# Kernel optimization log

Hardware: AMD Instinct MI355X
Metric: run time of the kernel (lower is better)

## Reference

```python
import jax, jax.numpy as jnp
import numpy as np

D_MODEL = 1024
D_STATE = 8          # max(8, 16 // 2)
D_CONV = 4
D_INNER = int(1.5 * D_MODEL)   # expand = max(1.5, 2*0.75)
DT_RANK = (D_MODEL + 15) // 16 # 64
D_FF = 2 * D_MODEL
B, L = 2, 2048


def layer_norm(x, g, b, eps=1e-5):
    mu = jnp.mean(x, -1, keepdims=True)
    var = jnp.var(x, -1, keepdims=True)
    return (x - mu) * jax.lax.rsqrt(var + eps) * g + b


def setup_inputs() -> dict:
    key = jax.random.key(0)
    ks = jax.random.split(key, 12)
    def n(k, shape, scale=0.02):
        return jax.random.normal(k, shape, dtype=jnp.float32) * scale
    return {
        'x': jax.random.normal(ks[0], (B, L, D_MODEL), dtype=jnp.float32),
        'ln1_g': jnp.ones((D_MODEL,), jnp.float32),
        'ln1_b': jnp.zeros((D_MODEL,), jnp.float32),
        'ln2_g': jnp.ones((D_MODEL,), jnp.float32),
        'ln2_b': jnp.zeros((D_MODEL,), jnp.float32),
        'in_proj_w': n(ks[1], (2 * D_INNER, D_MODEL)),
        'conv_w': n(ks[2], (D_INNER, 1, D_CONV), 0.1),
        'conv_b': jnp.zeros((D_INNER,), jnp.float32),
        'x_proj_w': n(ks[3], (DT_RANK + 2 * D_STATE, D_INNER)),
        'dt_proj_w': n(ks[4], (D_INNER, DT_RANK), 0.1),
        'dt_proj_b': n(ks[5], (D_INNER,), 0.1),
        'A_log': jnp.log(jnp.broadcast_to(jnp.arange(1, D_STATE + 1, dtype=jnp.float32), (D_INNER, D_STATE))),
        'D': jnp.ones((D_INNER,), jnp.float32),
        'out_proj_w': n(ks[6], (D_MODEL, D_INNER)),
        'ffn_w1': n(ks[7], (D_FF, D_MODEL)),
        'ffn_b1': jnp.zeros((D_FF,), jnp.float32),
        'ffn_w2': n(ks[8], (D_MODEL, D_FF)),
        'ffn_b2': jnp.zeros((D_MODEL,), jnp.float32),
    }


def mamba(x, in_proj_w, conv_w, conv_b, x_proj_w, dt_proj_w, dt_proj_b, A_log, Dp, out_proj_w):
    # in_proj -> (x, z)
    xz = x @ in_proj_w.T                       # (B, L, 2*d_inner)
    xi, z = jnp.split(xz, 2, axis=-1)
    # depthwise causal conv over seq, kernel 4
    xc = jnp.transpose(xi, (0, 2, 1))          # (B, d_inner, L)
    xc = jax.lax.conv_general_dilated(
        xc, conv_w, window_strides=(1,), padding=[(D_CONV - 1, 0)],
        dimension_numbers=('NCH', 'OIH', 'NCH'), feature_group_count=D_INNER)
    xc = xc + conv_b[None, :, None]
    u = jax.nn.silu(jnp.transpose(xc, (0, 2, 1)))  # (B, L, d_inner)
    # x_proj -> dt, B, C
    x_dbl = u @ x_proj_w.T
    dt = x_dbl[..., :DT_RANK]
    Bm = x_dbl[..., DT_RANK:DT_RANK + D_STATE]
    Cm = x_dbl[..., DT_RANK + D_STATE:]
    delta = jax.nn.softplus(dt @ dt_proj_w.T + dt_proj_b)  # (B, L, d_inner)
    A = -jnp.exp(A_log)                                    # (d_inner, d_state)
    dA = jnp.exp(jnp.einsum('bld,dn->bldn', delta, A))     # (B, L, d_inner, d_state)
    dBu = jnp.einsum('bld,bln,bld->bldn', delta, Bm, u)
    # selective scan over time
    def step(h, inputs):
        dA_t, dBu_t, C_t = inputs
        h = dA_t * h + dBu_t                   # (B, d_inner, d_state)
        y = jnp.einsum('bdn,bn->bd', h, C_t)
        return h, y
    h0 = jnp.zeros((x.shape[0], D_INNER, D_STATE), x.dtype)
    _, ys = jax.lax.scan(step, h0, (jnp.moveaxis(dA, 1, 0), jnp.moveaxis(dBu, 1, 0), jnp.moveaxis(Cm, 1, 0)))
    y = jnp.moveaxis(ys, 0, 1) + u * Dp        # skip connection D*u
    y = y * jax.nn.silu(z)                     # gate
    return y @ out_proj_w.T


def reference(x, ln1_g, ln1_b, ln2_g, ln2_b, in_proj_w, conv_w, conv_b, x_proj_w,
              dt_proj_w, dt_proj_b, A_log, D, out_proj_w, ffn_w1, ffn_b1, ffn_w2, ffn_b2):
    residual = x
    xp = layer_norm(x, ln1_g, ln1_b)
    x = mamba(xp, in_proj_w, conv_w, conv_b, x_proj_w, dt_proj_w, dt_proj_b, A_log, D, out_proj_w) + residual
    xn = layer_norm(x, ln2_g, ln2_b)
    h = jax.nn.gelu(xn @ ffn_w1.T + ffn_b1, approximate=False)  # dropout is identity in eval
    return x + (h @ ffn_w2.T + ffn_b2)
```

## Files before the change

### kernel.cpp

```cpp
#include <hip/hip_runtime.h>
#include <math.h>

#define D_MODEL 1024
#define D_STATE 8
#define D_CONV  4
#define D_INNER 1536
#define DT_RANK 64
#define D_FF    2048
#define BATCH   2
#define SEQ     2048
#define NROWS   (BATCH*SEQ)
#define NC      32
#define LC      (SEQ/NC)
#define XPAD    128

typedef short bf16x8 __attribute__((ext_vector_type(8)));
typedef unsigned short u16x8 __attribute__((ext_vector_type(8)));
typedef float f32x4  __attribute__((ext_vector_type(4)));

__device__ inline unsigned short f2bf(float x) {
    union { float f; unsigned u; } v; v.f = x;
    unsigned r = v.u + 0x7fffu + ((v.u >> 16) & 1u);
    return (unsigned short)(r >> 16);
}
__device__ inline float bf2f(unsigned short h) {
    union { unsigned u; float f; } v; v.u = ((unsigned)h) << 16;
    return v.f;
}
__device__ inline float softplus_f(float x) {
    return (x > 20.0f) ? x : log1pf(__expf(x));
}
__device__ inline float gelu_f(float x) {
    return 0.5f * x * (1.0f + erff(x * 0.70710678118654752f));
}
__device__ inline float silu_f(float x) {
    return x / (1.0f + __expf(-x));
}
__device__ inline void gload16(const unsigned short* g, unsigned short* l) {
    typedef unsigned int u32;
    __builtin_amdgcn_global_load_lds(
        (const __attribute__((address_space(1))) u32*)g,
        (__attribute__((address_space(3))) u32*)l, 16, 0, 0);
}

#define PHASE_SYNC_PRE()  do { __builtin_amdgcn_s_barrier(); \
                               asm volatile("s_waitcnt lgkmcnt(0)" ::: "memory"); } while (0)
#define PHASE_SYNC_POST() do { __builtin_amdgcn_s_barrier(); } while (0)

__global__ __launch_bounds__(256) void prep_kernel(
    const float* __restrict__ s0, unsigned short* __restrict__ d0,
    const float* __restrict__ s1, unsigned short* __restrict__ d1,
    const float* __restrict__ s2, unsigned short* __restrict__ d2,
    const float* __restrict__ s3, unsigned short* __restrict__ d3,
    const float* __restrict__ s4, unsigned short* __restrict__ d4,
    const float* __restrict__ xpw, unsigned short* __restrict__ xpd,
    const float* __restrict__ x, const float* __restrict__ g1,
    const float* __restrict__ b1, unsigned short* __restrict__ xout) {
    int b = blockIdx.x;
    if (b < 4400) {
        const float* s; unsigned short* d; int base;
        if      (b < 1536) { s = s0; d = d0; base = b * 2048; }
        else if (b < 1584) { s = s1; d = d1; base = (b - 1536) * 2048; }
        else if (b < 2352) { s = s2; d = d2; base = (b - 1584) * 2048; }
        else if (b < 3376) { s = s3; d = d3; base = (b - 2352) * 2048; }
        else               { s = s4; d = d4; base = (b - 3376) * 2048; }
        int i = base + threadIdx.x * 8;
        float4 v0 = *(const float4*)(s + i);
        float4 v1 = *(const float4*)(s + i + 4);
        ushort4 a, c;
        a.x = f2bf(v0.x); a.y = f2bf(v0.y); a.z = f2bf(v0.z); a.w = f2bf(v0.w);
        c.x = f2bf(v1.x); c.y = f2bf(v1.y); c.z = f2bf(v1.z); c.w = f2bf(v1.w);
        *(ushort4*)(d + i)     = a;
        *(ushort4*)(d + i + 4) = c;
    } else if (b < 4528) {
        int row = b - 4400;
        for (int c = threadIdx.x; c < D_INNER; c += 256)
            xpd[row * D_INNER + c] = (row < 80) ? f2bf(xpw[row * D_INNER + c]) : (unsigned short)0;
    } else {
        __shared__ float sbuf[4];
        int row = b - 4528;
        int t = threadIdx.x;
        float4 v = ((const float4*)(x + (size_t)row * D_MODEL))[t];
        float s = v.x + v.y + v.z + v.w;
        for (int o = 32; o; o >>= 1) s += __shfl_down(s, o, 64);
        if ((t & 63) == 0) sbuf[t >> 6] = s;
        __syncthreads();
        float mu = (sbuf[0] + sbuf[1] + sbuf[2] + sbuf[3]) * (1.0f / D_MODEL);
        __syncthreads();
        float e0 = v.x - mu, e1 = v.y - mu, e2 = v.z - mu, e3 = v.w - mu;
        float q = e0*e0 + e1*e1 + e2*e2 + e3*e3;
        for (int o = 32; o; o >>= 1) q += __shfl_down(q, o, 64);
        if ((t & 63) == 0) sbuf[t >> 6] = q;
        __syncthreads();
        float var = (sbuf[0] + sbuf[1] + sbuf[2] + sbuf[3]) * (1.0f / D_MODEL);
        float rs = rsqrtf(var + 1e-5f);
        float4 gv = ((const float4*)g1)[t];
        float4 bv = ((const float4*)b1)[t];
        ushort4 st;
        st.x = f2bf(e0 * rs * gv.x + bv.x);
        st.y = f2bf(e1 * rs * gv.y + bv.y);
        st.z = f2bf(e2 * rs * gv.z + bv.z);
        st.w = f2bf(e3 * rs * gv.w + bv.w);
        ((ushort4*)(xout + (size_t)row * D_MODEL))[t] = st;
    }
}

__global__ __launch_bounds__(256) void ln_kernel(const float* __restrict__ x,
                                                 const float* __restrict__ g,
                                                 const float* __restrict__ b,
                                                 unsigned short* __restrict__ out) {
    __shared__ float sbuf[4];
    int row = blockIdx.x;
    int t = threadIdx.x;
    float4 v = ((const float4*)(x + (size_t)row * D_MODEL))[t];
    float s = v.x + v.y + v.z + v.w;
    for (int o = 32; o; o >>= 1) s += __shfl_down(s, o, 64);
    if ((t & 63) == 0) sbuf[t >> 6] = s;
    __syncthreads();
    float mu = (sbuf[0] + sbuf[1] + sbuf[2] + sbuf[3]) * (1.0f / D_MODEL);
    __syncthreads();
    float d0 = v.x - mu, d1 = v.y - mu, d2 = v.z - mu, d3 = v.w - mu;
    float q = d0*d0 + d1*d1 + d2*d2 + d3*d3;
    for (int o = 32; o; o >>= 1) q += __shfl_down(q, o, 64);
    if ((t & 63) == 0) sbuf[t >> 6] = q;
    __syncthreads();
    float var = (sbuf[0] + sbuf[1] + sbuf[2] + sbuf[3]) * (1.0f / D_MODEL);
    float rs = rsqrtf(var + 1e-5f);
    float4 gv = ((const float4*)g)[t];
    float4 bv = ((const float4*)b)[t];
    ushort4 st;
    st.x = f2bf(d0 * rs * gv.x + bv.x);
    st.y = f2bf(d1 * rs * gv.y + bv.y);
    st.z = f2bf(d2 * rs * gv.z + bv.z);
    st.w = f2bf(d3 * rs * gv.w + bv.w);
    ((ushort4*)(out + (size_t)row * D_MODEL))[t] = st;
}

#define EPI_F32        0
#define EPI_F32_BF16   1
#define EPI_SOFTPLUS   2
#define EPI_RESID      3
#define EPI_GELU_BF16  4
#define EPI_BIAS_RESID 5
#define EPI_BF16       6
#define EPI_SOFTPLUS_BF16 7

template<int WN, int EPI, int SPLITK>
__global__ __launch_bounds__(512, 2) void gemm8p(
    const unsigned short* __restrict__ A, int lda,
    const unsigned short* __restrict__ Bm, int ldb, int K,
    float* __restrict__ Cf, unsigned short* __restrict__ Cb, int ldc,
    const float* __restrict__ bias,
    const float* __restrict__ resid, int ldr) {
    constexpr int WM = 8 / WN;
    constexpr int BN = WN * 64;
    constexpr int RW = 256 / WM;
    constexpr int CW = 64;
    constexpr int MI = RW / 16;
    constexpr int NI = CW / 16;
    constexpr int MIH = MI / 2, NIH = NI / 2;
    constexpr int ABYTES = 256 * 128;
    constexpr int BBYTES = BN * 128;
    constexpr int BOFF = 2 * ABYTES;
    __shared__ unsigned short lds[(2 * ABYTES + 2 * BBYTES) / 2];

    const int t = threadIdx.x, l = t & 63, w = t >> 6;
    const int wr = w / WN, wc = w % WN;

    const int nx = gridDim.x;
    const int nwg = nx * gridDim.y;
    int bid = blockIdx.y * nx + blockIdx.x;
    int q = nwg >> 3;
    int swz = (bid & 7) * q + (bid >> 3);
    const int m0 = (swz / nx) * 256, n0 = (swz % nx) * BN;
    const int kbase = (SPLITK > 1) ? blockIdx.z * K : 0;

    const int sr = l >> 3;
    const int sj = ((l & 7) * 16) ^ ((l >> 3) << 4);
    const int row_l = w * 8;
    const int row_c = (w >> 2) * 64 + (w & 3) * 8;

    auto STG = [&](int bufbyte, int rowbase, const unsigned short* G, int ldg, int gbase, int kt) {
        unsigned short* dst = (unsigned short*)((char*)lds + bufbyte + rowbase * 128);
        const unsigned short* src = G + (size_t)(gbase + rowbase + sr) * ldg + kbase + kt * 64 + (sj >> 1);
        gload16(src, dst);
    };
    auto S_Ah0 = [&](int b, int kt) {
        if (WN == 4) { STG(b * ABYTES, row_l, A, lda, m0, kt);       STG(b * ABYTES, 128 + row_l, A, lda, m0, kt); }
        else         { STG(b * ABYTES, row_c, A, lda, m0, kt);       STG(b * ABYTES, 128 + row_c, A, lda, m0, kt); }
    };
    auto S_Ah1 = [&](int b, int kt) {
        if (WN == 4) { STG(b * ABYTES, 64 + row_l, A, lda, m0, kt);  STG(b * ABYTES, 192 + row_l, A, lda, m0, kt); }
        else         { STG(b * ABYTES, 32 + row_c, A, lda, m0, kt);  STG(b * ABYTES, 160 + row_c, A, lda, m0, kt); }
    };
    auto S_Bc0 = [&](int b, int kt) {
        if (WN == 4) { STG(BOFF + b * BBYTES, row_c, Bm, ldb, n0, kt); STG(BOFF + b * BBYTES, 128 + row_c, Bm, ldb, n0, kt); }
        else         { STG(BOFF + b * BBYTES, row_c, Bm, ldb, n0, kt); }
    };
    auto S_Bc1 = [&](int b, int kt) {
        if (WN == 4) { STG(BOFF + b * BBYTES, 32 + row_c, Bm, ldb, n0, kt); STG(BOFF + b * BBYTES, 160 + row_c, Bm, ldb, n0, kt); }
        else         { STG(BOFF + b * BBYTES, 32 + row_c, Bm, ldb, n0, kt); }
    };

    auto LD = [&](int bytebase, int row, int kb) -> bf16x8 {
        int o = bytebase + row * 128 + (kb ^ ((row & 7) << 4));
        return *(const bf16x8*)((const char*)lds + o);
    };

    f32x4 acc[MI][NI] = {};
    bf16x8 af[MIH][2], b0v[NIH][2], b1v[NIH][2];

    auto LDA_set = [&](int buf, int qr, auto& dst) {
        #pragma unroll
        for (int mi = 0; mi < MIH; mi++)
            #pragma unroll
            for (int ks = 0; ks < 2; ks++)
                dst[mi][ks] = LD(buf * ABYTES, wr * RW + qr * (RW / 2) + mi * 16 + (l & 15),
                                 ks * 64 + (l >> 4) * 16);
    };
    auto LDB_set = [&](int buf, int qc, auto& dst) {
        #pragma unroll
        for (int ni2 = 0; ni2 < NIH; ni2++)
            #pragma unroll
            for (int ks = 0; ks < 2; ks++)
                dst[ni2][ks] = LD(BOFF + buf * BBYTES, wc * CW + qc * 32 + ni2 * 16 + (l & 15),
                                  ks * 64 + (l >> 4) * 16);
    };
    auto MFMA_Q = [&](int qr, int qc, auto& a_, auto& b_) {
        __builtin_amdgcn_s_setprio(1);
        #pragma unroll
        for (int mi = 0; mi < MIH; mi++)
            #pragma unroll
            for (int ni2 = 0; ni2 < NIH; ni2++)
                #pragma unroll
                for (int ks = 0; ks < 2; ks++)
                    acc[qr * MIH + mi][qc * NIH + ni2] =
                        __builtin_amdgcn_mfma_f32_16x16x32_bf16(a_[mi][ks], b_[ni2][ks],
                                                                acc[qr * MIH + mi][qc * NIH + ni2], 0, 0, 0);
        __builtin_amdgcn_s_setprio(0);
    };
    auto VMW = [&](bool last) {
        if (last)            asm volatile("s_waitcnt vmcnt(0)" ::: "memory");
        else if (WN == 4)    asm volatile("s_waitcnt vmcnt(6)" ::: "memory");
        else                 asm volatile("s_waitcnt vmcnt(5)" ::: "memory");
    };

    const int ni_ = K >> 7;

    S_Ah0(0, 0); S_Ah1(0, 0); S_Bc0(0, 0); S_Bc1(0, 0);
    S_Ah0(1, 1); S_Ah1(1, 1); S_Bc0(1, 1); S_Bc1(1, 1);
    if (WN == 4) asm volatile("s_waitcnt vmcnt(8)" ::: "memory");
    else         asm volatile("s_waitcnt vmcnt(6)" ::: "memory");
    __builtin_amdgcn_s_barrier();

    for (int i = 0; i < ni_; i++) {
        const bool last = (i == ni_ - 1);
        const int t2 = 2 * i + 2, t3 = 2 * i + 3;
        LDA_set(0, 0, af); LDB_set(0, 0, b0v);
        if (i) S_Bc0(1, 2 * i + 1);
        PHASE_SYNC_PRE(); MFMA_Q(0, 0, af, b0v); PHASE_SYNC_POST();
        LDB_set(0, 1, b1v);
        if (!last) S_Ah0(0, t2);
        PHASE_SYNC_PRE(); MFMA_Q(0, 1, af, b1v); PHASE_SYNC_POST();
        LDA_set(0, 1, af);
        PHASE_SYNC_PRE(); MFMA_Q(1, 1, af, b1v); PHASE_SYNC_POST();
        LDB_set(0, 0, b0v);
        if (!last) { S_Ah1(0, t2); S_Bc1(0, t2); }
        VMW(last);
        PHASE_SYNC_PRE(); MFMA_Q(1, 0, af, b0v); PHASE_SYNC_POST();
        LDA_set(1, 0, af); LDB_set(1, 0, b0v);
        if (!last) S_Bc0(0, t2);
        PHASE_SYNC_PRE(); MFMA_Q(0, 0, af, b0v); PHASE_SYNC_POST();
        LDB_set(1, 1, b1v);
        if (!last) S_Ah0(1, t3);
        PHASE_SYNC_PRE(); MFMA_Q(0, 1, af, b1v); PHASE_SYNC_POST();
        LDA_set(1, 1, af);
        PHASE_SYNC_PRE(); MFMA_Q(1, 1, af, b1v); PHASE_SYNC_POST();
        LDB_set(1, 0, b0v);
        if (!last) { S_Ah1(1, t3); S_Bc1(1, t3); }
        VMW(last);
        PHASE_SYNC_PRE(); MFMA_Q(1, 0, af, b0v); PHASE_SYNC_POST();
    }

    float* Cfp = Cf;
    if (SPLITK > 1) Cfp += (size_t)blockIdx.z * NROWS * ldc;
    #pragma unroll
    for (int ni2 = 0; ni2 < NI; ni2++) {
        int col = n0 + wc * CW + ni2 * 16 + (l & 15);
        float bv = 0.0f;
        if (EPI == EPI_SOFTPLUS || EPI == EPI_GELU_BF16 || EPI == EPI_BIAS_RESID) bv = bias[col];
        #pragma unroll
        for (int mi = 0; mi < MI; mi++) {
            #pragma unroll
            for (int j = 0; j < 4; j++) {
                int row = m0 + wr * RW + mi * 16 + (l >> 4) * 4 + j;
                float v = acc[mi][ni2][j];
                if (EPI == EPI_SOFTPLUS)        v = softplus_f(v + bv);
                else if (EPI == EPI_GELU_BF16)  v = gelu_f(v + bv);
                else if (EPI == EPI_RESID)      v = v + resid[(size_t)row * ldr + col];
                else if (EPI == EPI_BIAS_RESID) v = v + bv + resid[(size_t)row * ldr + col];
                if (EPI == EPI_GELU_BF16 || EPI == EPI_BF16) {
                    Cb[(size_t)row * ldc + col] = f2bf(v);
                } else {
                    Cfp[(size_t)row * ldc + col] = v;
                    if (EPI == EPI_F32_BF16) Cb[(size_t)row * ldc + col] = f2bf(v);
                }
            }
        }
    }
}

__global__ __launch_bounds__(256) void sk2_ln(const float* __restrict__ p,
                                              const float* __restrict__ resid,
                                              const float* __restrict__ g,
                                              const float* __restrict__ b,
                                              float* __restrict__ x2,
                                              unsigned short* __restrict__ xn) {
    __shared__ float sbuf[4];
    int row = blockIdx.x;
    int t = threadIdx.x;
    const size_t seg = (size_t)NROWS * D_MODEL;
    size_t base = (size_t)row * D_MODEL + t * 4;
    float4 a = *(const float4*)(p + base);
    float4 bb = *(const float4*)(p + base + seg);
    float4 r = *(const float4*)(resid + base);
    float4 v;
    v.x = a.x + bb.x + r.x;
    v.y = a.y + bb.y + r.y;
    v.z = a.z + bb.z + r.z;
    v.w = a.w + bb.w + r.w;
    *(float4*)(x2 + base) = v;
    float s = v.x + v.y + v.z + v.w;
    for (int o = 32; o; o >>= 1) s += __shfl_down(s, o, 64);
    if ((t & 63) == 0) sbuf[t >> 6] = s;
    __syncthreads();
    float mu = (sbuf[0] + sbuf[1] + sbuf[2] + sbuf[3]) * (1.0f / D_MODEL);
    __syncthreads();
    float d0 = v.x - mu, d1 = v.y - mu, d2 = v.z - mu, d3 = v.w - mu;
    float qq = d0*d0 + d1*d1 + d2*d2 + d3*d3;
    for (int o = 32; o; o >>= 1) qq += __shfl_down(qq, o, 64);
    if ((t & 63) == 0) sbuf[t >> 6] = qq;
    __syncthreads();
    float var = (sbuf[0] + sbuf[1] + sbuf[2] + sbuf[3]) * (1.0f / D_MODEL);
    float rs = rsqrtf(var + 1e-5f);
    float4 gv = ((const float4*)g)[t];
    float4 bv = ((const float4*)b)[t];
    ushort4 st;
    st.x = f2bf(d0 * rs * gv.x + bv.x);
    st.y = f2bf(d1 * rs * gv.y + bv.y);
    st.z = f2bf(d2 * rs * gv.z + bv.z);
    st.w = f2bf(d3 * rs * gv.w + bv.w);
    ((ushort4*)(xn + (size_t)row * D_MODEL))[t] = st;
}

__global__ __launch_bounds__(256) void sk2_reduce(const float* __restrict__ p,
                                                  const float* __restrict__ bias,
                                                  const float* __restrict__ resid,
                                                  float* __restrict__ o) {
    int i = (blockIdx.x * 256 + threadIdx.x) * 4;
    const size_t seg = (size_t)NROWS * D_MODEL;
    float4 a = *(const float4*)(p + i);
    float4 b = *(const float4*)(p + i + seg);
    float4 r = *(const float4*)(resid + i);
    float4 bb = *(const float4*)(bias + (i & (D_MODEL - 1)));
    float4 o4;
    o4.x = a.x + b.x + r.x + bb.x;
    o4.y = a.y + b.y + r.y + bb.y;
    o4.z = a.z + b.z + r.z + bb.z;
    o4.w = a.w + b.w + r.w + bb.w;
    *(float4*)(o + i) = o4;
}

template<int EPI, int SPLITK>
__global__ __launch_bounds__(256) void gemm_mfma(
    const unsigned short* __restrict__ A, int lda,
    const unsigned short* __restrict__ B, int ldb, int K,
    float* __restrict__ Cf, unsigned short* __restrict__ Cb, int ldc,
    const float* __restrict__ bias,
    const float* __restrict__ resid, int ldr) {
    __shared__ unsigned short As[3][128 * 32];
    __shared__ unsigned short Bs[3][128 * 32];
    int t = threadIdx.x, l = t & 63, w = t >> 6;
    int nx = gridDim.x;
    int nwg = nx * gridDim.y;
    int bid = blockIdx.y * nx + blockIdx.x;
    int q = nwg >> 3;
    int swz = (bid & 7) * q + (bid >> 3);
    int m0 = (swz / nx) * 128, n0 = (swz % nx) * 128;
    int kbase = (SPLITK > 1) ? blockIdx.z * K : 0;
    int c0 = 2 * w, c1 = 2 * w + 1;
    int srow = l >> 2, scol = (l & 3) * 8;
    const unsigned short* Ag0 = A + (size_t)(m0 + 16 * c0 + srow) * lda + kbase + scol;
    const unsigned short* Ag1 = A + (size_t)(m0 + 16 * c1 + srow) * lda + kbase + scol;
    const unsigned short* Bg0 = B + (size_t)(n0 + 16 * c0 + srow) * ldb + kbase + scol;
    const unsigned short* Bg1 = B + (size_t)(n0 + 16 * c1 + srow) * ldb + kbase + scol;
    int wr = w >> 1, wc = w & 1;
    int aoff = (wr * 64 + (l & 15)) * 32 + (l >> 4) * 8;
    int boff = (wc * 64 + (l & 15)) * 32 + (l >> 4) * 8;

    f32x4 acc[4][4] = {};
    int nt = K >> 5;

    gload16(Ag0, &As[0][c0 * 512]);
    gload16(Ag1, &As[0][c1 * 512]);
    gload16(Bg0, &Bs[0][c0 * 512]);
    gload16(Bg1, &Bs[0][c1 * 512]);
    if (nt > 1) {
        gload16(Ag0 + 32, &As[1][c0 * 512]);
        gload16(Ag1 + 32, &As[1][c1 * 512]);
        gload16(Bg0 + 32, &Bs[1][c0 * 512]);
        gload16(Bg1 + 32, &Bs[1][c1 * 512]);
    }

    int cur = 0;
    for (int ti = 0; ti < nt; ti++) {
        int pf = ti + 2;
        if (pf < nt) {
            int nb = cur - 1; if (nb < 0) nb += 3;
            int k0 = pf << 5;
            gload16(Ag0 + k0, &As[nb][c0 * 512]);
            gload16(Ag1 + k0, &As[nb][c1 * 512]);
            gload16(Bg0 + k0, &Bs[nb][c0 * 512]);
            gload16(Bg1 + k0, &Bs[nb][c1 * 512]);
        }
        int rem = nt - 1 - ti;
        if (rem >= 2)      asm volatile("s_waitcnt vmcnt(8)" ::: "memory");
        else if (rem == 1) asm volatile("s_waitcnt vmcnt(4)" ::: "memory");
        else               asm volatile("s_waitcnt vmcnt(0)" ::: "memory");
        __builtin_amdgcn_s_barrier();

        const unsigned short* Ab = &As[cur][0];
        const unsigned short* Bb = &Bs[cur][0];
        bf16x8 af[4], bfv[4];
        #pragma unroll
        for (int i = 0; i < 4; i++) af[i] = *(const bf16x8*)(Ab + aoff + i * 512);
        #pragma unroll
        for (int i = 0; i < 4; i++) bfv[i] = *(const bf16x8*)(Bb + boff + i * 512);
        __builtin_amdgcn_s_setprio(1);
        #pragma unroll
        for (int mi = 0; mi < 4; mi++)
            #pragma unroll
            for (int ni = 0; ni < 4; ni++)
                acc[mi][ni] = __builtin_amdgcn_mfma_f32_16x16x32_bf16(af[mi], bfv[ni], acc[mi][ni], 0, 0, 0);
        __builtin_amdgcn_s_setprio(0);
        __builtin_amdgcn_s_barrier();
        cur++; if (cur == 3) cur = 0;
    }

    if (SPLITK > 1) Cf += (size_t)blockIdx.z * NROWS * ldc;
    int colb = n0 + wc * 64 + (l & 15);
    int rowb = m0 + wr * 64 + (l >> 4) * 4;
    #pragma unroll
    for (int ni = 0; ni < 4; ni++) {
        int col = colb + ni * 16;
        float bv = 0.0f;
        if (EPI == EPI_SOFTPLUS || EPI == EPI_GELU_BF16 || EPI == EPI_BIAS_RESID || EPI == EPI_SOFTPLUS_BF16) bv = bias[col];
        #pragma unroll
        for (int mi = 0; mi < 4; mi++) {
            #pragma unroll
            for (int j = 0; j < 4; j++) {
                int row = rowb + mi * 16 + j;
                float v = acc[mi][ni][j];
                if (EPI == EPI_SOFTPLUS || EPI == EPI_SOFTPLUS_BF16) v = softplus_f(v + bv);
                else if (EPI == EPI_GELU_BF16)  v = gelu_f(v + bv);
                else if (EPI == EPI_RESID)      v = v + resid[(size_t)row * ldr + col];
                else if (EPI == EPI_BIAS_RESID) v = v + bv + resid[(size_t)row * ldr + col];
                if (EPI == EPI_GELU_BF16 || EPI == EPI_BF16 || EPI == EPI_SOFTPLUS_BF16) {
                    Cb[(size_t)row * ldc + col] = f2bf(v);
                } else {
                    Cf[(size_t)row * ldc + col] = v;
                    if (EPI == EPI_F32_BF16) Cb[(size_t)row * ldc + col] = f2bf(v);
                }
            }
        }
    }
}

__global__ __launch_bounds__(256) void xdbl_reduce(const float* __restrict__ part,
                                                   float* __restrict__ xdbl,
                                                   unsigned short* __restrict__ xdbl_bf) {
    int i = blockIdx.x * 256 + threadIdx.x;
    const size_t seg = (size_t)NROWS * XPAD;
    float s = part[i] + part[i + seg] + part[i + 2 * seg] + part[i + 3 * seg];
    xdbl[i] = s;
    xdbl_bf[i] = f2bf(s);
}

__global__ __launch_bounds__(256) void conv_silu(const unsigned short* __restrict__ xz,
                                                 const float* __restrict__ w,
                                                 const float* __restrict__ cb,
                                                 unsigned short* __restrict__ u) {
    int idx = (blockIdx.x * 256 + threadIdx.x) * 8;
    int d = idx % D_INNER;
    int bl = idx / D_INNER;
    int l = bl & (SEQ - 1);
    float acc[8];
    float4 wv[8];
    #pragma unroll
    for (int j = 0; j < 8; j++) wv[j] = *(const float4*)(w + (d + j) * 4);
    float4 cb0 = *(const float4*)(cb + d);
    float4 cb1 = *(const float4*)(cb + d + 4);
    acc[0] = cb0.x; acc[1] = cb0.y; acc[2] = cb0.z; acc[3] = cb0.w;
    acc[4] = cb1.x; acc[5] = cb1.y; acc[6] = cb1.z; acc[7] = cb1.w;
    #pragma unroll
    for (int k = 0; k < 4; k++) {
        int lp = l - 3 + k;
        if (lp >= 0) {
            u16x8 s = *(const u16x8*)(xz + (size_t)(bl - 3 + k) * (2 * D_INNER) + d);
            #pragma unroll
            for (int j = 0; j < 8; j++) {
                float wk = (k == 0) ? wv[j].x : (k == 1) ? wv[j].y : (k == 2) ? wv[j].z : wv[j].w;
                acc[j] += bf2f((unsigned short)s[j]) * wk;
            }
        }
    }
    u16x8 o;
    #pragma unroll
    for (int j = 0; j < 8; j++) o[j] = f2bf(silu_f(acc[j]));
    *(u16x8*)(u + idx) = o;
}

__global__ __launch_bounds__(256) void scan_passA(const unsigned short* __restrict__ delta,
                                                  const unsigned short* __restrict__ u,
                                                  const float* __restrict__ xdbl,
                                                  const float* __restrict__ A_log,
                                                  float* __restrict__ P,
                                                  float* __restrict__ S) {
    int d = blockIdx.x * 256 + threadIdx.x;
    int c = blockIdx.y, b = blockIdx.z;
    __shared__ float bc[LC][16];
    int base_row = b * SEQ + c * LC;
    for (int e = threadIdx.x; e < LC * 16; e += 256) {
        int lrr = e >> 4, col = e & 15;
        bc[lrr][col] = xdbl[(size_t)(base_row + lrr) * XPAD + DT_RANK + col];
    }
    __syncthreads();
    float Ad[8];
    #pragma unroll
    for (int n = 0; n < 8; n++) Ad[n] = -__expf(A_log[d * 8 + n]);
    float prod[8], hs[8];
    #pragma unroll
    for (int n = 0; n < 8; n++) { prod[n] = 1.0f; hs[n] = 0.0f; }
    for (int lrr = 0; lrr < LC; lrr++) {
        int row = base_row + lrr;
        float dl = bf2f(delta[(size_t)row * D_INNER + d]);
        float uu = bf2f(u[(size_t)row * D_INNER + d]);
        float du = dl * uu;
        #pragma unroll
        for (int n = 0; n < 8; n++) {
            float dA = __expf(dl * Ad[n]);
            prod[n] *= dA;
            hs[n] = dA * hs[n] + du * bc[lrr][n];
        }
    }
    size_t o = ((size_t)((size_t)b * NC + c) * D_INNER + d) * 8;
    #pragma unroll
    for (int n = 0; n < 8; n++) { P[o + n] = prod[n]; S[o + n] = hs[n]; }
}

__global__ __launch_bounds__(256) void scan_passB(const float* __restrict__ P,
                                                  const float* __restrict__ S,
                                                  float* __restrict__ hstart) {
    int tid = blockIdx.x * 256 + threadIdx.x;
    int b = tid / (D_INNER * 8);
    int rem = tid % (D_INNER * 8);
    float h = 0.0f;
    for (int c = 0; c < NC; c++) {
        size_t o = (size_t)(b * NC + c) * (D_INNER * 8) + rem;
        hstart[o] = h;
        h = P[o] * h + S[o];
    }
}

__global__ __launch_bounds__(256) void scan_passC(const unsigned short* __restrict__ delta,
                                                  const unsigned short* __restrict__ u,
                                                  const float* __restrict__ xdbl,
                                                  const float* __restrict__ A_log,
                                                  const float* __restrict__ hstart,
                                                  const unsigned short* __restrict__ xz,
                                                  const float* __restrict__ Dp,
                                                  unsigned short* __restrict__ ygate) {
    int d = blockIdx.x * 256 + threadIdx.x;
    int c = blockIdx.y, b = blockIdx.z;
    __shared__ float bc[LC][16];
    int base_row = b * SEQ + c * LC;
    for (int e = threadIdx.x; e < LC * 16; e += 256) {
        int lrr = e >> 4, col = e & 15;
        bc[lrr][col] = xdbl[(size_t)(base_row + lrr) * XPAD + DT_RANK + col];
    }
    __syncthreads();
    float Ad[8];
    #pragma unroll
    for (int n = 0; n < 8; n++) Ad[n] = -__expf(A_log[d * 8 + n]);
    float h[8];
    size_t ho = ((size_t)((size_t)b * NC + c) * D_INNER + d) * 8;
    #pragma unroll
    for (int n = 0; n < 8; n++) h[n] = hstart[ho + n];
    float Dd = Dp[d];
    for (int lrr = 0; lrr < LC; lrr++) {
        int row = base_row + lrr;
        float dl = bf2f(delta[(size_t)row * D_INNER + d]);
        float uu = bf2f(u[(size_t)row * D_INNER + d]);
        float du = dl * uu;
        float y = 0.0f;
        #pragma unroll
        for (int n = 0; n < 8; n++) {
            float dA = __expf(dl * Ad[n]);
            h[n] = dA * h[n] + du * bc[lrr][n];
            y += h[n] * bc[lrr][8 + n];
        }
        y += uu * Dd;
        float z = bf2f(xz[(size_t)row * (2 * D_INNER) + D_INNER + d]);
        ygate[(size_t)row * D_INNER + d] = f2bf(y * silu_f(z));
    }
}

extern "C" void kernel_launch(void* const* d_in, const int* in_sizes, int n_in,
                              void* d_out, int out_size, void* d_ws, size_t ws_size,
                              hipStream_t stream) {
    const float* x         = (const float*)d_in[0];
    const float* ln1_g     = (const float*)d_in[1];
    const float* ln1_b     = (const float*)d_in[2];
    const float* ln2_g     = (const float*)d_in[3];
    const float* ln2_b     = (const float*)d_in[4];
    const float* in_proj_w = (const float*)d_in[5];
    const float* conv_w    = (const float*)d_in[6];
    const float* conv_b    = (const float*)d_in[7];
    const float* x_proj_w  = (const float*)d_in[8];
    const float* dt_proj_w = (const float*)d_in[9];
    const float* dt_proj_b = (const float*)d_in[10];
    const float* A_log     = (const float*)d_in[11];
    const float* Dp        = (const float*)d_in[12];
    const float* out_proj_w= (const float*)d_in[13];
    const float* ffn_w1    = (const float*)d_in[14];
    const float* ffn_b1    = (const float*)d_in[15];
    const float* ffn_w2    = (const float*)d_in[16];
    const float* ffn_b2    = (const float*)d_in[17];
    float* out = (float*)d_out;

    float* xdbl  = (float*)d_ws;
    float* P     = xdbl + (size_t)NROWS * XPAD;
    float* S     = P + (size_t)BATCH * NC * D_INNER * 8;
    float* hst   = S + (size_t)BATCH * NC * D_INNER * 8;
    float* x2    = hst + (size_t)BATCH * NC * D_INNER * 8;
    float* psum  = x2 + (size_t)NROWS * D_MODEL;
    float* part  = psum;
    unsigned short* xz_bf   = (unsigned short*)(psum + 2 * (size_t)NROWS * D_MODEL);
    unsigned short* xp_bf   = xz_bf + (size_t)NROWS * 2 * D_INNER;
    unsigned short* u_bf    = xp_bf + (size_t)NROWS * D_MODEL;
    unsigned short* xdbl_bf = u_bf + (size_t)NROWS * D_INNER;
    unsigned short* yg_bf   = xdbl_bf + (size_t)NROWS * XPAD;
    unsigned short* dl_bf   = yg_bf + (size_t)NROWS * D_INNER;
    unsigned short* w_in    = dl_bf + (size_t)NROWS * D_INNER;
    unsigned short* w_xp    = w_in + (size_t)2 * D_INNER * D_MODEL;
    unsigned short* w_dt    = w_xp + (size_t)XPAD * D_INNER;
    unsigned short* w_out   = w_dt + (size_t)D_INNER * DT_RANK;
    unsigned short* w_f1    = w_out + (size_t)D_MODEL * D_INNER;
    unsigned short* w_f2    = w_f1 + (size_t)D_FF * D_MODEL;
    unsigned short* hff_bf  = xz_bf;

    prep_kernel<<<4400 + XPAD + NROWS, 256, 0, stream>>>(
        in_proj_w, w_in, dt_proj_w, w_dt, out_proj_w, w_out, ffn_w1, w_f1, ffn_w2, w_f2,
        x_proj_w, w_xp, x, ln1_g, ln1_b, xp_bf);
    gemm8p<4, EPI_BF16, 1><<<dim3(3072 / 256, NROWS / 256), 512, 0, stream>>>(
        xp_bf, D_MODEL, w_in, D_MODEL, D_MODEL, nullptr, xz_bf, 2 * D_INNER, nullptr, nullptr, 0);
    conv_silu<<<(NROWS * D_INNER) / (256 * 8), 256, 0, stream>>>(xz_bf, conv_w, conv_b, u_bf);
    gemm_mfma<EPI_F32, 4><<<dim3(1, NROWS / 128, 4), 256, 0, stream>>>(
        u_bf, D_INNER, w_xp, D_INNER, D_INNER / 4, part, nullptr, XPAD, nullptr, nullptr, 0);
    xdbl_reduce<<<(NROWS * XPAD) / 256, 256, 0, stream>>>(part, xdbl, xdbl_bf);
    gemm_mfma<EPI_SOFTPLUS_BF16, 1><<<dim3(D_INNER / 128, NROWS / 128), 256, 0, stream>>>(
        xdbl_bf, XPAD, w_dt, DT_RANK, DT_RANK, nullptr, dl_bf, D_INNER, dt_proj_b, nullptr, 0);
    scan_passA<<<dim3(D_INNER / 256, NC, BATCH), 256, 0, stream>>>(dl_bf, u_bf, xdbl, A_log, P, S);
    scan_passB<<<(BATCH * D_INNER * 8) / 256, 256, 0, stream>>>(P, S, hst);
    scan_passC<<<dim3(D_INNER / 256, NC, BATCH), 256, 0, stream>>>(dl_bf, u_bf, xdbl, A_log, hst, xz_bf, Dp, yg_bf);
    gemm8p<2, EPI_F32, 2><<<dim3(D_MODEL / 128, NROWS / 256, 2), 512, 0, stream>>>(
        yg_bf, D_INNER, w_out, D_INNER, D_INNER / 2, psum, nullptr, D_MODEL, nullptr, nullptr, 0);
    sk2_ln<<<NROWS, 256, 0, stream>>>(psum, x, ln2_g, ln2_b, x2, xp_bf);
    gemm8p<2, EPI_GELU_BF16, 1><<<dim3(D_FF / 128, NROWS / 256), 512, 0, stream>>>(
        xp_bf, D_MODEL, w_f1, D_MODEL, D_MODEL, nullptr, hff_bf, D_FF, ffn_b1, nullptr, 0);
    gemm8p<2, EPI_F32, 2><<<dim3(D_MODEL / 128, NROWS / 256, 2), 512, 0, stream>>>(
        hff_bf, D_FF, w_f2, D_FF, D_FF / 2, psum, nullptr, D_MODEL, nullptr, nullptr, 0);
    sk2_reduce<<<(NROWS * D_MODEL) / 1024, 256, 0, stream>>>(psum, ffn_b2, x2, out);
}
```

Before: 281.1 us.

## Use wider split-K GEMMs with bf16 tile-major partial scratch and separate reduce kernels

The out_proj and both FFN GEMMs now use 256x256 tiles with split-K of 4 or 2, including FFN1, which was not split before. Each split writes bf16 partials in a tile-major scratch layout with coalesced ushort4 stores. New skscr kernels sum the partials and apply the bias, GELU or residual epilogue. LayerNorm2 moves to the existing ln_kernel after the reduce. The aim is more parallelism and less partial-sum traffic, at the cost of bf16 rounding of partial sums and extra kernel launches.

```diff
diff --git a/kernel.cpp b/kernel.cpp
--- a/kernel.cpp
+++ b/kernel.cpp
@@ -137,12 +137,8 @@
 }
 
 #define EPI_F32        0
-#define EPI_F32_BF16   1
-#define EPI_SOFTPLUS   2
-#define EPI_RESID      3
-#define EPI_GELU_BF16  4
-#define EPI_BIAS_RESID 5
 #define EPI_BF16       6
+#define EPI_SCR        8
 #define EPI_SOFTPLUS_BF16 7
 
 template<int WN, int EPI, int SPLITK>
@@ -282,93 +278,91 @@
         PHASE_SYNC_PRE(); MFMA_Q(1, 0, af, b0v); PHASE_SYNC_POST();
     }
 
+    if (EPI == EPI_SCR) {
+        unsigned short* ps = Cb + (size_t)blockIdx.z * ((size_t)nwg * 65536);
+        size_t base = (size_t)swz * 65536 + w * 8192 + l * 4;
+        #pragma unroll
+        for (int mi = 0; mi < MI; mi++)
+            #pragma unroll
+            for (int ni2 = 0; ni2 < NI; ni2++) {
+                ushort4 pk;
+                pk.x = f2bf(acc[mi][ni2][0]);
+                pk.y = f2bf(acc[mi][ni2][1]);
+                pk.z = f2bf(acc[mi][ni2][2]);
+                pk.w = f2bf(acc[mi][ni2][3]);
+                *(ushort4*)(ps + base + (mi * 4 + ni2) * 256) = pk;
+            }
+        return;
+    }
+
     float* Cfp = Cf;
     if (SPLITK > 1) Cfp += (size_t)blockIdx.z * NROWS * ldc;
     #pragma unroll
     for (int ni2 = 0; ni2 < NI; ni2++) {
         int col = n0 + wc * CW + ni2 * 16 + (l & 15);
-        float bv = 0.0f;
-        if (EPI == EPI_SOFTPLUS || EPI == EPI_GELU_BF16 || EPI == EPI_BIAS_RESID) bv = bias[col];
         #pragma unroll
         for (int mi = 0; mi < MI; mi++) {
             #pragma unroll
             for (int j = 0; j < 4; j++) {
                 int row = m0 + wr * RW + mi * 16 + (l >> 4) * 4 + j;
                 float v = acc[mi][ni2][j];
-                if (EPI == EPI_SOFTPLUS)        v = softplus_f(v + bv);
-                else if (EPI == EPI_GELU_BF16)  v = gelu_f(v + bv);
-                else if (EPI == EPI_RESID)      v = v + resid[(size_t)row * ldr + col];
-                else if (EPI == EPI_BIAS_RESID) v = v + bv + resid[(size_t)row * ldr + col];
-                if (EPI == EPI_GELU_BF16 || EPI == EPI_BF16) {
+                if (EPI == EPI_BF16) {
                     Cb[(size_t)row * ldc + col] = f2bf(v);
                 } else {
                     Cfp[(size_t)row * ldc + col] = v;
-                    if (EPI == EPI_F32_BF16) Cb[(size_t)row * ldc + col] = f2bf(v);
                 }
             }
         }
     }
 }
 
-__global__ __launch_bounds__(256) void sk2_ln(const float* __restrict__ p,
-                                              const float* __restrict__ resid,
-                                              const float* __restrict__ g,
-                                              const float* __restrict__ b,
-                                              float* __restrict__ x2,
-                                              unsigned short* __restrict__ xn) {
-    __shared__ float sbuf[4];
-    int row = blockIdx.x;
-    int t = threadIdx.x;
-    const size_t seg = (size_t)NROWS * D_MODEL;
-    size_t base = (size_t)row * D_MODEL + t * 4;
-    float4 a = *(const float4*)(p + base);
-    float4 bb = *(const float4*)(p + base + seg);
-    float4 r = *(const float4*)(resid + base);
-    float4 v;
-    v.x = a.x + bb.x + r.x;
-    v.y = a.y + bb.y + r.y;
-    v.z = a.z + bb.z + r.z;
-    v.w = a.w + bb.w + r.w;
-    *(float4*)(x2 + base) = v;
-    float s = v.x + v.y + v.z + v.w;
-    for (int o = 32; o; o >>= 1) s += __shfl_down(s, o, 64);
-    if ((t & 63) == 0) sbuf[t >> 6] = s;
-    __syncthreads();
-    float mu = (sbuf[0] + sbuf[1] + sbuf[2] + sbuf[3]) * (1.0f / D_MODEL);
-    __syncthreads();
-    float d0 = v.x - mu, d1 = v.y - mu, d2 = v.z - mu, d3 = v.w - mu;
-    float qq = d0*d0 + d1*d1 + d2*d2 + d3*d3;
-    for (int o = 32; o; o >>= 1) qq += __shfl_down(qq, o, 64);
-    if ((t & 63) == 0) sbuf[t >> 6] = qq;
-    __syncthreads();
-    float var = (sbuf[0] + sbuf[1] + sbuf[2] + sbuf[3]) * (1.0f / D_MODEL);
-    float rs = rsqrtf(var + 1e-5f);
-    float4 gv = ((const float4*)g)[t];
-    float4 bv = ((const float4*)b)[t];
-    ushort4 st;
-    st.x = f2bf(d0 * rs * gv.x + bv.x);
-    st.y = f2bf(d1 * rs * gv.y + bv.y);
-    st.z = f2bf(d2 * rs * gv.z + bv.z);
-    st.w = f2bf(d3 * rs * gv.w + bv.w);
-    ((ushort4*)(xn + (size_t)row * D_MODEL))[t] = st;
-}
-
-__global__ __launch_bounds__(256) void sk2_reduce(const float* __restrict__ p,
-                                                  const float* __restrict__ bias,
-                                                  const float* __restrict__ resid,
-                                                  float* __restrict__ o) {
-    int i = (blockIdx.x * 256 + threadIdx.x) * 4;
-    const size_t seg = (size_t)NROWS * D_MODEL;
-    float4 a = *(const float4*)(p + i);
-    float4 b = *(const float4*)(p + i + seg);
-    float4 r = *(const float4*)(resid + i);
-    float4 bb = *(const float4*)(bias + (i & (D_MODEL - 1)));
-    float4 o4;
-    o4.x = a.x + b.x + r.x + bb.x;
-    o4.y = a.y + b.y + r.y + bb.y;
-    o4.z = a.z + b.z + r.z + bb.z;
-    o4.w = a.w + b.w + r.w + bb.w;
-    *(float4*)(o + i) = o4;
+template<int MODE>
+__global__ __launch_bounds__(256) void skscr(const unsigned short* __restrict__ ps,
+                                             const float* __restrict__ bias,
+                                             const float* __restrict__ resid,
+                                             float* __restrict__ of,
+                                             unsigned short* __restrict__ ob,
+                                             int nchunks, int N) {
+    int tid = blockIdx.x * 256 + threadIdx.x;
+    int c = tid >> 14;
+    int r = tid & 16383;
+    int w = r >> 11;
+    int f = (r >> 6) & 31;
+    int l = r & 63;
+    int mi = f >> 2, ni2 = f & 3;
+    int nx = N >> 8;
+    int m0 = (c / nx) << 8, n0 = (c % nx) << 8;
+    int row = m0 + ((w >> 2) << 7) + mi * 16 + ((l >> 4) << 2);
+    int col = n0 + ((w & 3) << 6) + ni2 * 16 + (l & 15);
+    size_t off = (size_t)c * 65536 + w * 8192 + f * 256 + l * 4;
+    size_t seg = (size_t)nchunks * 65536;
+    ushort4 a0 = *(const ushort4*)(ps + off);
+    ushort4 a1 = *(const ushort4*)(ps + off + seg);
+    float v0 = bf2f(a0.x) + bf2f(a1.x);
+    float v1 = bf2f(a0.y) + bf2f(a1.y);
+    float v2 = bf2f(a0.z) + bf2f(a1.z);
+    float v3 = bf2f(a0.w) + bf2f(a1.w);
+    if (MODE != 1) {
+        ushort4 a2 = *(const ushort4*)(ps + off + 2 * seg);
+        ushort4 a3 = *(const ushort4*)(ps + off + 3 * seg);
+        v0 += bf2f(a2.x) + bf2f(a3.x);
+        v1 += bf2f(a2.y) + bf2f(a3.y);
+        v2 += bf2f(a2.z) + bf2f(a3.z);
+        v3 += bf2f(a2.w) + bf2f(a3.w);
+    }
+    float bv = (MODE != 0) ? bias[col] : 0.0f;
+    float vv[4] = {v0, v1, v2, v3};
+    #pragma unroll
+    for (int j = 0; j < 4; j++) {
+        size_t o = (size_t)(row + j) * N + col;
+        if (MODE == 1) {
+            ob[o] = f2bf(gelu_f(vv[j] + bv));
+        } else if (MODE == 0) {
+            of[o] = vv[j] + resid[o];
+        } else {
+            of[o] = vv[j] + bv + resid[o];
+        }
+    }
 }
 
 template<int EPI, int SPLITK>
@@ -454,22 +448,18 @@
     for (int ni = 0; ni < 4; ni++) {
         int col = colb + ni * 16;
         float bv = 0.0f;
-        if (EPI == EPI_SOFTPLUS || EPI == EPI_GELU_BF16 || EPI == EPI_BIAS_RESID || EPI == EPI_SOFTPLUS_BF16) bv = bias[col];
+        if (EPI == EPI_SOFTPLUS_BF16) bv = bias[col];
         #pragma unroll
         for (int mi = 0; mi < 4; mi++) {
             #pragma unroll
             for (int j = 0; j < 4; j++) {
                 int row = rowb + mi * 16 + j;
                 float v = acc[mi][ni][j];
-                if (EPI == EPI_SOFTPLUS || EPI == EPI_SOFTPLUS_BF16) v = softplus_f(v + bv);
-                else if (EPI == EPI_GELU_BF16)  v = gelu_f(v + bv);
-                else if (EPI == EPI_RESID)      v = v + resid[(size_t)row * ldr + col];
-                else if (EPI == EPI_BIAS_RESID) v = v + bv + resid[(size_t)row * ldr + col];
-                if (EPI == EPI_GELU_BF16 || EPI == EPI_BF16 || EPI == EPI_SOFTPLUS_BF16) {
+                if (EPI == EPI_SOFTPLUS_BF16) v = softplus_f(v + bv);
+                if (EPI == EPI_BF16 || EPI == EPI_SOFTPLUS_BF16) {
                     Cb[(size_t)row * ldc + col] = f2bf(v);
                 } else {
                     Cf[(size_t)row * ldc + col] = v;
-                    if (EPI == EPI_F32_BF16) Cb[(size_t)row * ldc + col] = f2bf(v);
                 }
             }
         }
@@ -643,9 +633,10 @@
     float* S     = P + (size_t)BATCH * NC * D_INNER * 8;
     float* hst   = S + (size_t)BATCH * NC * D_INNER * 8;
     float* x2    = hst + (size_t)BATCH * NC * D_INNER * 8;
-    float* psum  = x2 + (size_t)NROWS * D_MODEL;
-    float* part  = psum;
-    unsigned short* xz_bf   = (unsigned short*)(psum + 2 * (size_t)NROWS * D_MODEL);
+    float* psumf = x2 + (size_t)NROWS * D_MODEL;
+    float* part  = psumf;
+    unsigned short* psum = (unsigned short*)psumf;
+    unsigned short* xz_bf   = (unsigned short*)(psumf + 2 * (size_t)NROWS * D_MODEL);
     unsigned short* xp_bf   = xz_bf + (size_t)NROWS * 2 * D_INNER;
     unsigned short* u_bf    = xp_bf + (size_t)NROWS * D_MODEL;
     unsigned short* xdbl_bf = u_bf + (size_t)NROWS * D_INNER;
@@ -673,12 +664,14 @@
     scan_passA<<<dim3(D_INNER / 256, NC, BATCH), 256, 0, stream>>>(dl_bf, u_bf, xdbl, A_log, P, S);
     scan_passB<<<(BATCH * D_INNER * 8) / 256, 256, 0, stream>>>(P, S, hst);
     scan_passC<<<dim3(D_INNER / 256, NC, BATCH), 256, 0, stream>>>(dl_bf, u_bf, xdbl, A_log, hst, xz_bf, Dp, yg_bf);
-    gemm8p<2, EPI_F32, 2><<<dim3(D_MODEL / 128, NROWS / 256, 2), 512, 0, stream>>>(
-        yg_bf, D_INNER, w_out, D_INNER, D_INNER / 2, psum, nullptr, D_MODEL, nullptr, nullptr, 0);
-    sk2_ln<<<NROWS, 256, 0, stream>>>(psum, x, ln2_g, ln2_b, x2, xp_bf);
-    gemm8p<2, EPI_GELU_BF16, 1><<<dim3(D_FF / 128, NROWS / 256), 512, 0, stream>>>(
-        xp_bf, D_MODEL, w_f1, D_MODEL, D_MODEL, nullptr, hff_bf, D_FF, ffn_b1, nullptr, 0);
-    gemm8p<2, EPI_F32, 2><<<dim3(D_MODEL / 128, NROWS / 256, 2), 512, 0, stream>>>(
-        hff_bf, D_FF, w_f2, D_FF, D_FF / 2, psum, nullptr, D_MODEL, nullptr, nullptr, 0);
-    sk2_reduce<<<(NROWS * D_MODEL) / 1024, 256, 0, stream>>>(psum, ffn_b2, x2, out);
-}
+    gemm8p<4, EPI_SCR, 4><<<dim3(D_MODEL / 256, NROWS / 256, 4), 512, 0, stream>>>(
+        yg_bf, D_INNER, w_out, D_INNER, D_INNER / 4, nullptr, psum, D_MODEL, nullptr, nullptr, 0);
+    skscr<0><<<(64 * 16384) / 256, 256, 0, stream>>>(psum, nullptr, x, x2, nullptr, 64, D_MODEL);
+    ln_kernel<<<NROWS, 256, 0, stream>>>(x2, ln2_g, ln2_b, xp_bf);
+    gemm8p<4, EPI_SCR, 2><<<dim3(D_FF / 256, NROWS / 256, 2), 512, 0, stream>>>(
+        xp_bf, D_MODEL, w_f1, D_MODEL, D_MODEL / 2, nullptr, psum, D_FF, nullptr, nullptr, 0);
+    skscr<1><<<(128 * 16384) / 256, 256, 0, stream>>>(psum, ffn_b1, nullptr, nullptr, hff_bf, 128, D_FF);
+    gemm8p<4, EPI_SCR, 4><<<dim3(D_MODEL / 256, NROWS / 256, 4), 512, 0, stream>>>(
+        hff_bf, D_FF, w_f2, D_FF, D_FF / 4, nullptr, psum, D_MODEL, nullptr, nullptr, 0);
+    skscr<2><<<(64 * 16384) / 256, 256, 0, stream>>>(psum, ffn_b2, x2, out, nullptr, 64, D_MODEL);
+}
```

Result: slower. 290.2 us (+3.2%).
